# Optimization experiments

Measured on AMD Instinct MI355X. Metric: run time of the kernel, lower is better.

Reference implementation:

```python
import jax, jax.numpy as jnp
import numpy as np

B, L, C, H, K = 4096, 64, 7, 32, 2  # batch, series length, input ch, hidden ch, RK4 substeps per knot


def _linear_params(k, out_d, in_d):
    bound = 1.0 / np.sqrt(in_d)
    kw, kb = jax.random.split(k)
    W = jax.random.uniform(kw, (out_d, in_d), minval=-bound, maxval=bound, dtype=jnp.float32)
    b = jax.random.uniform(kb, (out_d,), minval=-bound, maxval=bound, dtype=jnp.float32)
    return W, b


def setup_inputs() -> dict:
    key = jax.random.key(0)
    ks = jax.random.split(key, 6)
    cde_src = jax.random.normal(ks[0], (B, L, C), dtype=jnp.float32)
    W_init, b_init = _linear_params(ks[1], H, C)          # initial: Linear(C, H)
    Wf1, bf1 = _linear_params(ks[2], 32, H)               # func.linear1: Linear(H, 32)
    Wf2, bf2 = _linear_params(ks[3], C * H, 32)           # func.linear2: Linear(32, C*H)
    Wo1, bo1 = _linear_params(ks[4], 16, H)               # linear1: Linear(H, 16)
    Wo2, bo2 = _linear_params(ks[5], 3, 16)               # linear2: Linear(16, 3)
    return {"cde_src": cde_src, "W_init": W_init, "b_init": b_init,
            "Wf1": Wf1, "bf1": bf1, "Wf2": Wf2, "bf2": bf2,
            "Wo1": Wo1, "bo1": bo1, "Wo2": Wo2, "bo2": bo2}


def reference(cde_src, W_init, b_init, Wf1, bf1, Wf2, bf2, Wo1, bo1, Wo2, bo2):
    x = cde_src  # (B, L, C); uniform times t = 0..L-1 (torchcde default), so dt = 1
    # Hermite cubic coefficients with backward differences (torchcde), dt = 1:
    diffs = x[:, 1:] - x[:, :-1]                       # (B, L-1, C) backward differences
    d = jnp.concatenate([diffs[:, :1], diffs], axis=1)  # derivative at each knot
    m0, m1 = d[:, :-1], d[:, 1:]
    cb = m0                                            # 'b' coeff (= dX/dt at left knot)
    two_c = 2.0 * (3.0 * diffs - 2.0 * m0 - m1)        # (B, L-1, C)
    three_d = 3.0 * (-2.0 * diffs + m0 + m1)           # (B, L-1, C)

    z0 = x[:, 0] @ W_init.T + b_init                   # initial(X(t0))  -> (B, H)

    def dXdt(t):
        idx = jnp.clip(jnp.floor(t), 0, L - 2).astype(jnp.int32)
        f = t - idx.astype(t.dtype)
        return cb[:, idx] + (two_c[:, idx] + three_d[:, idx] * f) * f  # (B, C)

    def vf(t, z):
        h1 = jax.nn.softplus(z @ Wf1.T + bf1)                    # (B, 32)
        g = jnp.tanh(h1 @ Wf2.T + bf2).reshape(z.shape[0], H, C)  # (B, H, C)
        return jnp.einsum('bhc,bc->bh', g, dXdt(t))

    h = 1.0 / K
    times = jnp.arange((L - 1) * K, dtype=jnp.float32) * h

    def step(z, t):
        k1 = vf(t, z)
        k2 = vf(t + 0.5 * h, z + (0.5 * h) * k1)
        k3 = vf(t + 0.5 * h, z + (0.5 * h) * k2)
        k4 = vf(t + h, z + h * k3)
        return z + (h / 6.0) * (k1 + 2.0 * k2 + 2.0 * k3 + k4), None

    zT, _ = jax.lax.scan(step, z0, times)  # z at final time (== zT[:, 1] in torch)
    out = jax.nn.softplus(zT @ Wo1.T + bo1) @ Wo2.T + bo2  # (B, 3)
    return out
```

## Files before the change

kernel.cpp:

```cpp
#include <hip/hip_runtime.h>
#include <hip/hip_bf16.h>
#include <stdint.h>

typedef __bf16 bf16_t;
typedef __bf16 bf16x8 __attribute__((ext_vector_type(8)));
typedef float f32x4 __attribute__((ext_vector_type(4)));

#define LOG2E 1.44269504088896340736f
#define LN2 0.69314718055994530942f

__device__ __forceinline__ float fast_exp2(float x) { return __builtin_amdgcn_exp2f(x); }
__device__ __forceinline__ float fast_log2(float x) { return __builtin_amdgcn_logf(x); }
__device__ __forceinline__ float fast_rcp(float x) { return __builtin_amdgcn_rcpf(x); }

__device__ __forceinline__ float softplus_f(float x) {
    float sp = LN2 * fast_log2(1.0f + fast_exp2(x * LOG2E));
    return (x > 20.0f) ? x : sp;
}
__device__ __forceinline__ float tanh_f(float x) {
    float e = fast_exp2(x * (2.0f * LOG2E));
    return 1.0f - 2.0f * fast_rcp(1.0f + e);
}

__device__ __forceinline__ uint32_t cvt_bf16(float a) {
    uint32_t r;
    asm("v_cvt_pk_bf16_f32 %0, %1, %2" : "=v"(r) : "v"(a), "v"(a));
    return r;
}

template <int CTRL>
__device__ __forceinline__ float dpp_add(float v) {
    int iv = __builtin_bit_cast(int, v);
    int sv = __builtin_amdgcn_update_dpp(0, iv, CTRL, 0xF, 0xF, true);
    return v + __builtin_bit_cast(float, sv);
}
__device__ __forceinline__ float red8(float v) {
    v = dpp_add<0xB1>(v);
    v = dpp_add<0x4E>(v);
    v = dpp_add<0x141>(v);
    return v;
}

__global__ __launch_bounds__(512, 2) void cde_kernel(
    const float* __restrict__ x,
    const float* __restrict__ Wi,
    const float* __restrict__ bi,
    const float* __restrict__ W1,
    const float* __restrict__ b1,
    const float* __restrict__ W2,
    const float* __restrict__ b2,
    const float* __restrict__ Wo1,
    const float* __restrict__ bo1,
    const float* __restrict__ Wo2,
    const float* __restrict__ bo2,
    float* __restrict__ out)
{
    __shared__ float diffs[16][441];
    __shared__ float dxsT[8][20];
    __shared__ uint16_t zhiu[4][16][8], zlou[4][16][8];
    __shared__ uint16_t h1hiu[4][16][8], h1lou[4][16][8];
    __shared__ float zfin[16][32];
    __shared__ float wo1t[32][16];
    __shared__ float ubuf[16][16];

    const int tid = threadIdx.x;
    const int l = tid & 63;
    const int w = tid >> 6;
    const int r0 = blockIdx.x * 16;

    const int ar = l & 15;
    const int chunk = l >> 4;
    const int ak = chunk * 8;
    const int crow = chunk * 4;

    const int T1 = w >> 2, reg1 = w & 3;
    const int h1col = 16 * T1 + ar;

    const int group = l >> 3;
    const int g = l & 7;
    const int dT = g >> 2, drr = g & 3;
    const int dcol = 4 * w + 2 * dT + (group & 1);
    const int drow = crow + drr;
    const bool selb0 = (drr & 1) != 0;
    const bool selb1 = (drr & 2) != 0;
    const bool selbT = dT != 0;

    const bf16x8* pZh = (const bf16x8*)&zhiu[chunk][ar][0];
    const bf16x8* pZl = (const bf16x8*)&zlou[chunk][ar][0];
    const bf16x8* pHh = (const bf16x8*)&h1hiu[chunk][ar][0];
    const bf16x8* pHl = (const bf16x8*)&h1lou[chunk][ar][0];
    const f32x4* pDx = (const f32x4*)&dxsT[g][crow];
    uint16_t* pH1wh = &h1hiu[h1col >> 3][crow + reg1][h1col & 7];
    uint16_t* pH1wl = &h1lou[h1col >> 3][crow + reg1][h1col & 7];
    uint16_t* pZwh = &zhiu[dcol >> 3][drow][dcol & 7];
    uint16_t* pZwl = &zlou[dcol >> 3][drow][dcol & 7];

    bf16x8 w1h, w1l;
    {
        const float* p = &W1[h1col * 32 + ak];
#pragma unroll
        for (int j = 0; j < 8; ++j) {
            float v = p[j];
            bf16_t hh = (bf16_t)v;
            w1h[j] = hh;
            w1l[j] = (bf16_t)(v - (float)hh);
        }
    }
    const float b1c = b1[h1col];

    bf16x8 w2h[2], w2l[2];
    float b2c[2];
#pragma unroll
    for (int T = 0; T < 2; ++T) {
        int N = 32 * w + 16 * T + ar;
        int hcol = N >> 3, ccol = N & 7;
        if (ccol < 7) {
            const float* p = &W2[(hcol * 7 + ccol) * 32 + ak];
#pragma unroll
            for (int j = 0; j < 8; ++j) {
                float v = p[j];
                bf16_t hh = (bf16_t)v;
                w2h[T][j] = hh;
                w2l[T][j] = (bf16_t)(v - (float)hh);
            }
            b2c[T] = b2[hcol * 7 + ccol];
        } else {
#pragma unroll
            for (int j = 0; j < 8; ++j) { w2h[T][j] = (bf16_t)0.0f; w2l[T][j] = (bf16_t)0.0f; }
            b2c[T] = 0.0f;
        }
    }

    for (int e = tid; e < 16 * 441; e += 512) {
        int r = e / 441, rem = e - r * 441;
        const float* px = &x[(size_t)(r0 + r) * 448];
        diffs[r][rem] = px[rem + 7] - px[rem];
    }
    {
        int r = tid >> 5, hh = tid & 31;
        const float* px = &x[(size_t)(r0 + r) * 448];
        float acc = bi[hh];
#pragma unroll
        for (int c = 0; c < 7; ++c) acc += px[c] * Wi[hh * 7 + c];
        zfin[r][hh] = acc;
        uint32_t zh = cvt_bf16(acc);
        float zhf = __builtin_bit_cast(float, zh << 16);
        uint32_t zl = cvt_bf16(acc - zhf);
        zhiu[hh >> 3][r][hh & 7] = (uint16_t)zh;
        zlou[hh >> 3][r][hh & 7] = (uint16_t)zl;
    }
    if (tid < 16) dxsT[7][tid] = 0.0f;
    __syncthreads();

    float zb = zfin[drow][dcol];
    float ka = 0.0f;

    for (int k = 0; k < 126; ++k) {
#pragma unroll
        for (int s = 0; s < 4; ++s) {
            if (s != 2 && (l & 31) < 7) {
                int rdx = w + ((l >> 5) << 3);
                int cdx = l & 31;
                int m = 2 * k + (s == 0 ? 0 : (s == 3 ? 2 : 1));
                int i = m >> 2; if (i > 62) i = 62;
                float f = 0.25f * (float)(m - 4 * i);
                float D = diffs[rdx][i * 7 + cdx];
                float a = diffs[rdx][(i > 0 ? i - 1 : 0) * 7 + cdx];
                dxsT[cdx][rdx] = a + (D - a) * (f * (4.0f - 3.0f * f));
            }
            {
                bf16x8 azh = *pZh;
                bf16x8 azl = *pZl;
                f32x4 d1 = {b1c, b1c, b1c, b1c};
                d1 = __builtin_amdgcn_mfma_f32_16x16x32_bf16(azh, w1h, d1, 0, 0, 0);
                d1 = __builtin_amdgcn_mfma_f32_16x16x32_bf16(azl, w1h, d1, 0, 0, 0);
                d1 = __builtin_amdgcn_mfma_f32_16x16x32_bf16(azh, w1l, d1, 0, 0, 0);
                float sp = softplus_f(d1[reg1]);
                uint32_t shu = cvt_bf16(sp);
                float shf = __builtin_bit_cast(float, shu << 16);
                uint32_t slu = cvt_bf16(sp - shf);
                *pH1wh = (uint16_t)shu;
                *pH1wl = (uint16_t)slu;
            }
            __syncthreads();
            {
                bf16x8 ahh = *pHh;
                bf16x8 ahl = *pHl;
                f32x4 dxv = *pDx;
                float vsel0, vsel1;
#pragma unroll
                for (int T = 0; T < 2; ++T) {
                    f32x4 d2 = {b2c[T], b2c[T], b2c[T], b2c[T]};
                    d2 = __builtin_amdgcn_mfma_f32_16x16x32_bf16(ahh, w2h[T], d2, 0, 0, 0);
                    d2 = __builtin_amdgcn_mfma_f32_16x16x32_bf16(ahl, w2h[T], d2, 0, 0, 0);
                    d2 = __builtin_amdgcn_mfma_f32_16x16x32_bf16(ahh, w2l[T], d2, 0, 0, 0);
                    float vr0 = red8(tanh_f(d2[0]) * dxv[0]);
                    float vr1 = red8(tanh_f(d2[1]) * dxv[1]);
                    float vr2 = red8(tanh_f(d2[2]) * dxv[2]);
                    float vr3 = red8(tanh_f(d2[3]) * dxv[3]);
                    float t01 = selb0 ? vr1 : vr0;
                    float t23 = selb0 ? vr3 : vr2;
                    float ts = selb1 ? t23 : t01;
                    if (T == 0) vsel0 = ts; else vsel1 = ts;
                }
                float v = selbT ? vsel1 : vsel0;
                float zs;
                if (s == 0)      { ka = v;           zs = zb + 0.25f * v; }
                else if (s == 1) { ka += 2.0f * v;   zs = zb + 0.25f * v; }
                else if (s == 2) { ka += 2.0f * v;   zs = zb + 0.5f * v; }
                else             { zb += (1.0f / 12.0f) * (ka + v); zs = zb; }
                uint32_t zhu = cvt_bf16(zs);
                float zhf = __builtin_bit_cast(float, zhu << 16);
                uint32_t zlu = cvt_bf16(zs - zhf);
                *pZwh = (uint16_t)zhu;
                *pZwl = (uint16_t)zlu;
            }
            __syncthreads();
        }
    }

    zfin[drow][dcol] = zb;
    {
        int hh = tid >> 4, jj = tid & 15;
        wo1t[hh][jj] = Wo1[jj * 32 + hh];
    }
    __syncthreads();
    if (tid < 256) {
        int r = tid >> 4, jj = tid & 15;
        float acc = bo1[jj];
#pragma unroll
        for (int hh = 0; hh < 32; ++hh) acc += zfin[r][hh] * wo1t[hh][jj];
        ubuf[r][jj] = softplus_f(acc);
    }
    __syncthreads();
    if (tid < 48) {
        int r = tid / 3, o = tid - (tid / 3) * 3;
        float acc = bo2[o];
#pragma unroll
        for (int j = 0; j < 16; ++j) acc += ubuf[r][j] * Wo2[o * 16 + j];
        out[(size_t)(r0 + r) * 3 + o] = acc;
    }
}

extern "C" void kernel_launch(void* const* d_in, const int* in_sizes, int n_in,
                              void* d_out, int out_size, void* d_ws, size_t ws_size,
                              hipStream_t stream) {
    (void)in_sizes; (void)n_in; (void)d_ws; (void)ws_size; (void)out_size;
    const float* x   = (const float*)d_in[0];
    const float* Wi  = (const float*)d_in[1];
    const float* bi  = (const float*)d_in[2];
    const float* W1  = (const float*)d_in[3];
    const float* b1  = (const float*)d_in[4];
    const float* W2  = (const float*)d_in[5];
    const float* b2  = (const float*)d_in[6];
    const float* Wo1 = (const float*)d_in[7];
    const float* bo1 = (const float*)d_in[8];
    const float* Wo2 = (const float*)d_in[9];
    const float* bo2 = (const float*)d_in[10];
    cde_kernel<<<dim3(256), dim3(512), 0, stream>>>(x, Wi, bi, W1, b1, W2, b2,
                                                    Wo1, bo1, Wo2, bo2, (float*)d_out);
}
```

Baseline: 469.2 us.

## Halve block to 4 waves, doubling per-wave work and folding log2e into weights

Cuts the workgroup from 8 waves to 4. Each wave now computes four second-layer MFMA tiles and owns two z elements per lane, and the first-layer MFMAs run as three independent accumulators summed afterwards. The nested step loop is flattened, and the LOG2E / 2*LOG2E scale is folded into W1, b1, W2 and b2 so softplus and tanh skip a multiply. The aim is cheaper barriers and more instruction-level parallelism per wave, at the cost of fewer waves to hide latency and more registers per thread.

```diff
diff --git a/kernel.cpp b/kernel.cpp
--- a/kernel.cpp
+++ b/kernel.cpp
@@ -13,12 +13,12 @@
 __device__ __forceinline__ float fast_log2(float x) { return __builtin_amdgcn_logf(x); }
 __device__ __forceinline__ float fast_rcp(float x) { return __builtin_amdgcn_rcpf(x); }
 
-__device__ __forceinline__ float softplus_f(float x) {
-    float sp = LN2 * fast_log2(1.0f + fast_exp2(x * LOG2E));
-    return (x > 20.0f) ? x : sp;
-}
-__device__ __forceinline__ float tanh_f(float x) {
-    float e = fast_exp2(x * (2.0f * LOG2E));
+__device__ __forceinline__ float softplus_t(float t) {
+    float sp = LN2 * fast_log2(1.0f + fast_exp2(t));
+    return (t > 28.9f) ? t * LN2 : sp;
+}
+__device__ __forceinline__ float tanh_t(float t) {
+    float e = fast_exp2(t);
     return 1.0f - 2.0f * fast_rcp(1.0f + e);
 }
 
@@ -26,6 +26,13 @@
     uint32_t r;
     asm("v_cvt_pk_bf16_f32 %0, %1, %2" : "=v"(r) : "v"(a), "v"(a));
     return r;
+}
+__device__ __forceinline__ void pack_bf16(float v, uint16_t* ph, uint16_t* pl) {
+    uint32_t h = cvt_bf16(v);
+    float hf = __builtin_bit_cast(float, h << 16);
+    uint32_t lo = cvt_bf16(v - hf);
+    *ph = (uint16_t)h;
+    *pl = (uint16_t)lo;
 }
 
 template <int CTRL>
@@ -41,7 +48,7 @@
     return v;
 }
 
-__global__ __launch_bounds__(512, 2) void cde_kernel(
+__global__ __launch_bounds__(256, 1) void cde_kernel(
     const float* __restrict__ x,
     const float* __restrict__ Wi,
     const float* __restrict__ bi,
@@ -72,165 +79,188 @@
     const int chunk = l >> 4;
     const int ak = chunk * 8;
     const int crow = chunk * 4;
-
-    const int T1 = w >> 2, reg1 = w & 3;
+    const int g = l & 7;
+
+    const int T1 = w >> 1;
+    const int rA = 2 * (w & 1);
     const int h1col = 16 * T1 + ar;
-
-    const int group = l >> 3;
-    const int g = l & 7;
-    const int dT = g >> 2, drr = g & 3;
-    const int dcol = 4 * w + 2 * dT + (group & 1);
-    const int drow = crow + drr;
-    const bool selb0 = (drr & 1) != 0;
-    const bool selb1 = (drr & 2) != 0;
-    const bool selbT = dT != 0;
+    const bool lowpair = (w & 1) == 0;
+
+    const int hb = (l >> 3) & 1;
+    const int dcol = 8 * w + 2 * (g >> 1) + hb;
+    const int drow0 = crow + 2 * (g & 1);
+    const int drow1 = drow0 + 1;
+    const bool selr = (g & 1) != 0;
+    const bool sj1 = (g & 2) != 0;
+    const bool sj2 = (g & 4) != 0;
 
     const bf16x8* pZh = (const bf16x8*)&zhiu[chunk][ar][0];
     const bf16x8* pZl = (const bf16x8*)&zlou[chunk][ar][0];
     const bf16x8* pHh = (const bf16x8*)&h1hiu[chunk][ar][0];
     const bf16x8* pHl = (const bf16x8*)&h1lou[chunk][ar][0];
     const f32x4* pDx = (const f32x4*)&dxsT[g][crow];
-    uint16_t* pH1wh = &h1hiu[h1col >> 3][crow + reg1][h1col & 7];
-    uint16_t* pH1wl = &h1lou[h1col >> 3][crow + reg1][h1col & 7];
-    uint16_t* pZwh = &zhiu[dcol >> 3][drow][dcol & 7];
-    uint16_t* pZwl = &zlou[dcol >> 3][drow][dcol & 7];
+    uint16_t* pH0h = &h1hiu[h1col >> 3][crow + rA][h1col & 7];
+    uint16_t* pH0l = &h1lou[h1col >> 3][crow + rA][h1col & 7];
+    uint16_t* pH1h = &h1hiu[h1col >> 3][crow + rA + 1][h1col & 7];
+    uint16_t* pH1l = &h1lou[h1col >> 3][crow + rA + 1][h1col & 7];
+    uint16_t* pZ0h = &zhiu[dcol >> 3][drow0][dcol & 7];
+    uint16_t* pZ0l = &zlou[dcol >> 3][drow0][dcol & 7];
+    uint16_t* pZ1h = &zhiu[dcol >> 3][drow1][dcol & 7];
+    uint16_t* pZ1l = &zlou[dcol >> 3][drow1][dcol & 7];
 
     bf16x8 w1h, w1l;
     {
         const float* p = &W1[h1col * 32 + ak];
 #pragma unroll
         for (int j = 0; j < 8; ++j) {
-            float v = p[j];
+            float v = p[j] * LOG2E;
             bf16_t hh = (bf16_t)v;
             w1h[j] = hh;
             w1l[j] = (bf16_t)(v - (float)hh);
         }
     }
-    const float b1c = b1[h1col];
-
-    bf16x8 w2h[2], w2l[2];
-    float b2c[2];
-#pragma unroll
-    for (int T = 0; T < 2; ++T) {
-        int N = 32 * w + 16 * T + ar;
-        int hcol = N >> 3, ccol = N & 7;
-        if (ccol < 7) {
+    const float b1c = b1[h1col] * LOG2E;
+
+    bf16x8 w2h[4], w2l[4];
+    float b2c[4];
+    const bool cvalid = (ar & 7) < 7;
+#pragma unroll
+    for (int j = 0; j < 4; ++j) {
+        int hcol = 8 * w + 2 * j + (ar >> 3);
+        int ccol = ar & 7;
+        if (cvalid) {
             const float* p = &W2[(hcol * 7 + ccol) * 32 + ak];
 #pragma unroll
-            for (int j = 0; j < 8; ++j) {
-                float v = p[j];
+            for (int q = 0; q < 8; ++q) {
+                float v = p[q] * (2.0f * LOG2E);
                 bf16_t hh = (bf16_t)v;
-                w2h[T][j] = hh;
-                w2l[T][j] = (bf16_t)(v - (float)hh);
+                w2h[j][q] = hh;
+                w2l[j][q] = (bf16_t)(v - (float)hh);
             }
-            b2c[T] = b2[hcol * 7 + ccol];
+            b2c[j] = b2[hcol * 7 + ccol] * (2.0f * LOG2E);
         } else {
 #pragma unroll
-            for (int j = 0; j < 8; ++j) { w2h[T][j] = (bf16_t)0.0f; w2l[T][j] = (bf16_t)0.0f; }
-            b2c[T] = 0.0f;
-        }
-    }
-
-    for (int e = tid; e < 16 * 441; e += 512) {
+            for (int q = 0; q < 8; ++q) { w2h[j][q] = (bf16_t)0.0f; w2l[j][q] = (bf16_t)0.0f; }
+            b2c[j] = 0.0f;
+        }
+    }
+
+    for (int e = tid; e < 16 * 441; e += 256) {
         int r = e / 441, rem = e - r * 441;
         const float* px = &x[(size_t)(r0 + r) * 448];
         diffs[r][rem] = px[rem + 7] - px[rem];
     }
-    {
-        int r = tid >> 5, hh = tid & 31;
+#pragma unroll
+    for (int e0 = 0; e0 < 2; ++e0) {
+        int e = tid + e0 * 256;
+        int r = e >> 5, hh = e & 31;
         const float* px = &x[(size_t)(r0 + r) * 448];
         float acc = bi[hh];
 #pragma unroll
         for (int c = 0; c < 7; ++c) acc += px[c] * Wi[hh * 7 + c];
         zfin[r][hh] = acc;
-        uint32_t zh = cvt_bf16(acc);
-        float zhf = __builtin_bit_cast(float, zh << 16);
-        uint32_t zl = cvt_bf16(acc - zhf);
-        zhiu[hh >> 3][r][hh & 7] = (uint16_t)zh;
-        zlou[hh >> 3][r][hh & 7] = (uint16_t)zl;
+        pack_bf16(acc, &zhiu[hh >> 3][r][hh & 7], &zlou[hh >> 3][r][hh & 7]);
     }
     if (tid < 16) dxsT[7][tid] = 0.0f;
     __syncthreads();
 
-    float zb = zfin[drow][dcol];
-    float ka = 0.0f;
-
-    for (int k = 0; k < 126; ++k) {
-#pragma unroll
-        for (int s = 0; s < 4; ++s) {
-            if (s != 2 && (l & 31) < 7) {
-                int rdx = w + ((l >> 5) << 3);
-                int cdx = l & 31;
-                int m = 2 * k + (s == 0 ? 0 : (s == 3 ? 2 : 1));
-                int i = m >> 2; if (i > 62) i = 62;
-                float f = 0.25f * (float)(m - 4 * i);
-                float D = diffs[rdx][i * 7 + cdx];
-                float a = diffs[rdx][(i > 0 ? i - 1 : 0) * 7 + cdx];
-                dxsT[cdx][rdx] = a + (D - a) * (f * (4.0f - 3.0f * f));
+    float zb0 = zfin[drow0][dcol];
+    float zb1 = zfin[drow1][dcol];
+    float ka0 = 0.0f, ka1 = 0.0f;
+
+    for (int it = 0; it < 504; ++it) {
+        const int s = it & 3;
+        const int k = it >> 2;
+
+        if (s != 2 && (l & 15) < 7) {
+            int rdx = w + 4 * (l >> 4);
+            int cdx = l & 15;
+            int m = 2 * k + (s == 0 ? 0 : (s == 3 ? 2 : 1));
+            int i = m >> 2; if (i > 62) i = 62;
+            float f = 0.25f * (float)(m - 4 * i);
+            float D = diffs[rdx][i * 7 + cdx];
+            float a = diffs[rdx][(i > 0 ? i - 1 : 0) * 7 + cdx];
+            dxsT[cdx][rdx] = a + (D - a) * (f * (4.0f - 3.0f * f));
+        }
+        {
+            bf16x8 azh = *pZh;
+            bf16x8 azl = *pZl;
+            f32x4 zero4 = {0.0f, 0.0f, 0.0f, 0.0f};
+            f32x4 b14 = {b1c, b1c, b1c, b1c};
+            f32x4 d1a = __builtin_amdgcn_mfma_f32_16x16x32_bf16(azh, w1h, b14, 0, 0, 0);
+            f32x4 d1b = __builtin_amdgcn_mfma_f32_16x16x32_bf16(azl, w1h, zero4, 0, 0, 0);
+            f32x4 d1c = __builtin_amdgcn_mfma_f32_16x16x32_bf16(azh, w1l, zero4, 0, 0, 0);
+            float y0 = (lowpair ? d1a[0] : d1a[2]) + (lowpair ? d1b[0] : d1b[2]) +
+                       (lowpair ? d1c[0] : d1c[2]);
+            float y1 = (lowpair ? d1a[1] : d1a[3]) + (lowpair ? d1b[1] : d1b[3]) +
+                       (lowpair ? d1c[1] : d1c[3]);
+            pack_bf16(softplus_t(y0), pH0h, pH0l);
+            pack_bf16(softplus_t(y1), pH1h, pH1l);
+        }
+        __syncthreads();
+
+        {
+            bf16x8 ahh = *pHh;
+            bf16x8 ahl = *pHl;
+            f32x4 dxv = *pDx;
+            float vr[4][4];
+#pragma unroll
+            for (int j = 0; j < 4; ++j) {
+                f32x4 d2 = {b2c[j], b2c[j], b2c[j], b2c[j]};
+                d2 = __builtin_amdgcn_mfma_f32_16x16x32_bf16(ahh, w2h[j], d2, 0, 0, 0);
+                d2 = __builtin_amdgcn_mfma_f32_16x16x32_bf16(ahl, w2h[j], d2, 0, 0, 0);
+                d2 = __builtin_amdgcn_mfma_f32_16x16x32_bf16(ahh, w2l[j], d2, 0, 0, 0);
+#pragma unroll
+                for (int r = 0; r < 4; ++r)
+                    vr[j][r] = red8(tanh_t(d2[r]) * dxv[r]);
             }
-            {
-                bf16x8 azh = *pZh;
-                bf16x8 azl = *pZl;
-                f32x4 d1 = {b1c, b1c, b1c, b1c};
-                d1 = __builtin_amdgcn_mfma_f32_16x16x32_bf16(azh, w1h, d1, 0, 0, 0);
-                d1 = __builtin_amdgcn_mfma_f32_16x16x32_bf16(azl, w1h, d1, 0, 0, 0);
-                d1 = __builtin_amdgcn_mfma_f32_16x16x32_bf16(azh, w1l, d1, 0, 0, 0);
-                float sp = softplus_f(d1[reg1]);
-                uint32_t shu = cvt_bf16(sp);
-                float shf = __builtin_bit_cast(float, shu << 16);
-                uint32_t slu = cvt_bf16(sp - shf);
-                *pH1wh = (uint16_t)shu;
-                *pH1wl = (uint16_t)slu;
+            float u0 = selr ? vr[0][2] : vr[0][0];
+            float u1 = selr ? vr[1][2] : vr[1][0];
+            float u2 = selr ? vr[2][2] : vr[2][0];
+            float u3 = selr ? vr[3][2] : vr[3][0];
+            float va = sj2 ? (sj1 ? u3 : u2) : (sj1 ? u1 : u0);
+            float q0 = selr ? vr[0][3] : vr[0][1];
+            float q1 = selr ? vr[1][3] : vr[1][1];
+            float q2 = selr ? vr[2][3] : vr[2][1];
+            float q3 = selr ? vr[3][3] : vr[3][1];
+            float vb = sj2 ? (sj1 ? q3 : q2) : (sj1 ? q1 : q0);
+
+            float zs0, zs1;
+            if (s == 0) {
+                ka0 = va; ka1 = vb;
+                zs0 = zb0 + 0.25f * va; zs1 = zb1 + 0.25f * vb;
+            } else if (s == 1) {
+                ka0 += 2.0f * va; ka1 += 2.0f * vb;
+                zs0 = zb0 + 0.25f * va; zs1 = zb1 + 0.25f * vb;
+            } else if (s == 2) {
+                ka0 += 2.0f * va; ka1 += 2.0f * vb;
+                zs0 = zb0 + 0.5f * va; zs1 = zb1 + 0.5f * vb;
+            } else {
+                zb0 += (1.0f / 12.0f) * (ka0 + va);
+                zb1 += (1.0f / 12.0f) * (ka1 + vb);
+                zs0 = zb0; zs1 = zb1;
             }
-            __syncthreads();
-            {
-                bf16x8 ahh = *pHh;
-                bf16x8 ahl = *pHl;
-                f32x4 dxv = *pDx;
-                float vsel0, vsel1;
-#pragma unroll
-                for (int T = 0; T < 2; ++T) {
-                    f32x4 d2 = {b2c[T], b2c[T], b2c[T], b2c[T]};
-                    d2 = __builtin_amdgcn_mfma_f32_16x16x32_bf16(ahh, w2h[T], d2, 0, 0, 0);
-                    d2 = __builtin_amdgcn_mfma_f32_16x16x32_bf16(ahl, w2h[T], d2, 0, 0, 0);
-                    d2 = __builtin_amdgcn_mfma_f32_16x16x32_bf16(ahh, w2l[T], d2, 0, 0, 0);
-                    float vr0 = red8(tanh_f(d2[0]) * dxv[0]);
-                    float vr1 = red8(tanh_f(d2[1]) * dxv[1]);
-                    float vr2 = red8(tanh_f(d2[2]) * dxv[2]);
-                    float vr3 = red8(tanh_f(d2[3]) * dxv[3]);
-                    float t01 = selb0 ? vr1 : vr0;
-                    float t23 = selb0 ? vr3 : vr2;
-                    float ts = selb1 ? t23 : t01;
-                    if (T == 0) vsel0 = ts; else vsel1 = ts;
-                }
-                float v = selbT ? vsel1 : vsel0;
-                float zs;
-                if (s == 0)      { ka = v;           zs = zb + 0.25f * v; }
-                else if (s == 1) { ka += 2.0f * v;   zs = zb + 0.25f * v; }
-                else if (s == 2) { ka += 2.0f * v;   zs = zb + 0.5f * v; }
-                else             { zb += (1.0f / 12.0f) * (ka + v); zs = zb; }
-                uint32_t zhu = cvt_bf16(zs);
-                float zhf = __builtin_bit_cast(float, zhu << 16);
-                uint32_t zlu = cvt_bf16(zs - zhf);
-                *pZwh = (uint16_t)zhu;
-                *pZwl = (uint16_t)zlu;
-            }
-            __syncthreads();
-        }
-    }
-
-    zfin[drow][dcol] = zb;
+            pack_bf16(zs0, pZ0h, pZ0l);
+            pack_bf16(zs1, pZ1h, pZ1l);
+        }
+        __syncthreads();
+    }
+
+    zfin[drow0][dcol] = zb0;
+    zfin[drow1][dcol] = zb1;
+#pragma unroll
+    for (int e0 = 0; e0 < 2; ++e0) {
+        int e = tid + e0 * 256;
+        int hh = e >> 4, jj = e & 15;
+        wo1t[hh][jj] = Wo1[jj * 32 + hh];
+    }
+    __syncthreads();
     {
-        int hh = tid >> 4, jj = tid & 15;
-        wo1t[hh][jj] = Wo1[jj * 32 + hh];
-    }
-    __syncthreads();
-    if (tid < 256) {
         int r = tid >> 4, jj = tid & 15;
         float acc = bo1[jj];
 #pragma unroll
         for (int hh = 0; hh < 32; ++hh) acc += zfin[r][hh] * wo1t[hh][jj];
-        ubuf[r][jj] = softplus_f(acc);
+        ubuf[r][jj] = softplus_t(acc * LOG2E);
     }
     __syncthreads();
     if (tid < 48) {
@@ -257,6 +287,6 @@
     const float* bo1 = (const float*)d_in[8];
     const float* Wo2 = (const float*)d_in[9];
     const float* bo2 = (const float*)d_in[10];
-    cde_kernel<<<dim3(256), dim3(512), 0, stream>>>(x, Wi, bi, W1, b1, W2, b2,
+    cde_kernel<<<dim3(256), dim3(256), 0, stream>>>(x, Wi, bi, W1, b1, W2, b2,
                                                     Wo1, bo1, Wo2, bo2, (float*)d_out);
 }
```

Result: slower. 548.1 us (+16.8%).
